# Kernel tuning notes

Measured on AMD Instinct MI355X. Metric: run time of the kernel, lower is better.

The kernel has to match this reference:

```python
import jax, jax.numpy as jnp
import numpy as np
import math

B, T, C = 2, 2048, 1024
H = 16            # n_head
RATIO = 4         # ratio_kv
HKV = H // RATIO  # n_head_kv = 4
HD = C // H       # head_dim = 64
G = H // HKV      # query heads per kv head = 4


def _alibi_slopes(n_heads):
    # n_heads must be a power of 2 here (H=16)
    assert math.log2(n_heads).is_integer()
    start = 2.0 ** (-(2.0 ** (-(math.log2(n_heads) - 3))))
    return np.array([start * (start ** i) for i in range(n_heads)], dtype=np.float32)


def setup_inputs() -> dict:
    key = jax.random.key(0)
    ks = jax.random.split(key, 5)
    return {
        "x": jax.random.normal(ks[0], (B, T, C), dtype=jnp.float32),
        "Wq": jax.random.normal(ks[1], (C, C), dtype=jnp.float32) * 0.02,
        "Wk": jax.random.normal(ks[2], (C, HKV * HD), dtype=jnp.float32) * 0.02,
        "Wv": jax.random.normal(ks[3], (C, HKV * HD), dtype=jnp.float32) * 0.02,
        "Wo": jax.random.normal(ks[4], (C, C), dtype=jnp.float32) * 0.02,
    }


def reference(x, Wq, Wk, Wv, Wo):
    # GQA causal attention with ALiBi bias (flash-disabled fallback path).
    # q: [B,HKV,G,T,HD] (grouped query heads), k/v: [B,HKV,T,HD]
    q = (x @ Wq).reshape(B, T, H, HD).transpose(0, 2, 1, 3).reshape(B, HKV, G, T, HD)
    k = (x @ Wk).reshape(B, T, HKV, HD).transpose(0, 2, 1, 3)
    v = (x @ Wv).reshape(B, T, HKV, HD).transpose(0, 2, 1, 3)

    scale = 1.0 / math.sqrt(HD)
    att = jnp.einsum('bkgtd,bksd->bkgts', q, k) * scale  # [B,HKV,G,T,T]

    # ALiBi: original repeats alibi(n_head) by G and truncates to n_head,
    # so query head h uses slope get_slopes(H)[h // G] == slopes[:HKV] per kv group.
    slopes = jnp.asarray(_alibi_slopes(H))[:HKV]          # [HKV]
    pos = jnp.arange(T)
    rel = (pos[None, :] - pos[:, None]).astype(jnp.float32)  # [T,T], rel[i,j]=j-i
    bias = slopes[:, None, None] * rel                    # [HKV,T,T]
    causal = jnp.triu(jnp.full((T, T), -jnp.inf, dtype=jnp.float32), 1)

    att = att + bias[None, :, None] + causal
    att = jax.nn.softmax(att.astype(jnp.float32), axis=-1).astype(q.dtype)

    y = jnp.einsum('bkgts,bksd->bkgtd', att, v)           # [B,HKV,G,T,HD]
    y = y.reshape(B, H, T, HD).transpose(0, 2, 1, 3).reshape(B, T, C)
    return y @ Wo
```

## Files before the change

### kernel.cpp

```cpp
#include <hip/hip_runtime.h>
#include <hip/hip_bf16.h>
#include <math.h>

#define B_ 2
#define T_ 2048
#define C_ 1024
#define H_ 16
#define HKV_ 4
#define G_ 4
#define HD_ 64
#define KVC_ 256
#define NQKV_ 1536
#define NQT_ 32

typedef __attribute__((ext_vector_type(8))) short bf16x8;
typedef __attribute__((ext_vector_type(4))) float f32x4;

static __device__ inline short f2bf(float f) {
    __hip_bfloat16 h = __float2bfloat16(f);
    short s;
    __builtin_memcpy(&s, &h, 2);
    return s;
}
static __device__ inline short f2bf_trunc(float f) {
    unsigned int u;
    __builtin_memcpy(&u, &f, 4);
    return (short)(u >> 16);
}
static __device__ inline float bf2f(short s) {
    unsigned int u = ((unsigned int)(unsigned short)s) << 16;
    float f;
    __builtin_memcpy(&f, &u, 4);
    return f;
}

static __device__ inline void gload_lds16(const short* g, short* lds) {
    __builtin_amdgcn_global_load_lds(
        (const __attribute__((address_space(1))) unsigned int*)g,
        (__attribute__((address_space(3))) unsigned int*)lds, 16, 0, 0);
}

__global__ __launch_bounds__(256) void cast_bf16(
    const float* __restrict__ in, short* __restrict__ out, int n)
{
    const int i = (blockIdx.x * 256 + threadIdx.x) * 8;
    if (i >= n) return;
    const float4 a = *(const float4*)(in + i);
    const float4 b = *(const float4*)(in + i + 4);
    bf16x8 o;
    o[0] = f2bf(a.x); o[1] = f2bf(a.y); o[2] = f2bf(a.z); o[3] = f2bf(a.w);
    o[4] = f2bf(b.x); o[5] = f2bf(b.y); o[6] = f2bf(b.z); o[7] = f2bf(b.w);
    *(bf16x8*)(out + i) = o;
}

__global__ __launch_bounds__(256) void w_transpose(
    const float* __restrict__ Wq, const float* __restrict__ Wk,
    const float* __restrict__ Wv, const float* __restrict__ Wo,
    short* __restrict__ Wt, short* __restrict__ Wot)
{
    const int z = blockIdx.z;
    const float* in;
    short* out;
    int N;
    if (z == 0)      { in = Wq; out = Wt;                     N = C_; }
    else if (z == 1) { in = Wk; out = Wt + C_ * C_;           N = KVC_; }
    else if (z == 2) { in = Wv; out = Wt + (C_ + KVC_) * C_;  N = KVC_; }
    else             { in = Wo; out = Wot;                    N = C_; }
    const int n0 = blockIdx.x * 32;
    if (n0 >= N) return;
    __shared__ float t[32][33];
    const int tx = threadIdx.x, ty = threadIdx.y;
    const int k0 = blockIdx.y * 32;
    #pragma unroll
    for (int j = 0; j < 4; j++)
        t[ty + j * 8][tx] = in[(size_t)(k0 + ty + j * 8) * N + n0 + tx];
    __syncthreads();
    #pragma unroll
    for (int j = 0; j < 4; j++)
        out[(size_t)(n0 + ty + j * 8) * C_ + k0 + tx] = f2bf(t[tx][ty + j * 8]);
}

template <bool OUT_BF16>
__global__ __launch_bounds__(256) void gemm_bf16(
    const short* __restrict__ A, const short* __restrict__ Bt,
    void* __restrict__ Cout, int M, int N, int K)
{
    __shared__ short As[64 * 32];
    __shared__ short Bs[128 * 32];
    const int tid = threadIdx.x;
    const int wave = tid >> 6, lane = tid & 63;
    const int l15 = lane & 15, quad = lane >> 4;
    const int row0 = blockIdx.y * 64, col0 = blockIdx.x * 128;
    const int wrow = (wave >> 1) * 32, wcol = (wave & 1) * 64;

    f32x4 acc[2][4];
    #pragma unroll
    for (int i = 0; i < 2; i++)
        #pragma unroll
        for (int j = 0; j < 4; j++)
            acc[i][j] = (f32x4){0.f, 0.f, 0.f, 0.f};

    for (int kt = 0; kt < K; kt += 32) {
        __syncthreads();
        {
            const int r = wave * 16 + (lane >> 2);
            const int kof = (lane & 3) * 8;
            gload_lds16(A + (size_t)(row0 + r) * K + kt + kof, &As[wave * 512]);
        }
        #pragma unroll
        for (int c2 = 0; c2 < 2; c2++) {
            const int c = wave * 2 + c2;
            const int r = c * 16 + (lane >> 2);
            const int kof = (lane & 3) * 8;
            gload_lds16(Bt + (size_t)(col0 + r) * K + kt + kof, &Bs[c * 512]);
        }
        __syncthreads();

        bf16x8 af[2], bf[4];
        #pragma unroll
        for (int mt = 0; mt < 2; mt++)
            af[mt] = *(const bf16x8*)&As[(wrow + mt * 16 + l15) * 32 + quad * 8];
        #pragma unroll
        for (int nt = 0; nt < 4; nt++)
            bf[nt] = *(const bf16x8*)&Bs[(wcol + nt * 16 + l15) * 32 + quad * 8];
        #pragma unroll
        for (int mt = 0; mt < 2; mt++)
            #pragma unroll
            for (int nt = 0; nt < 4; nt++)
                acc[mt][nt] = __builtin_amdgcn_mfma_f32_16x16x32_bf16(
                    af[mt], bf[nt], acc[mt][nt], 0, 0, 0);
    }

    #pragma unroll
    for (int mt = 0; mt < 2; mt++) {
        #pragma unroll
        for (int r = 0; r < 4; r++) {
            const size_t row = row0 + wrow + mt * 16 + quad * 4 + r;
            #pragma unroll
            for (int nt = 0; nt < 4; nt++) {
                const size_t col = col0 + wcol + nt * 16 + l15;
                if (OUT_BF16)
                    ((short*)Cout)[row * N + col] = f2bf(acc[mt][nt][r]);
                else
                    ((float*)Cout)[row * N + col] = acc[mt][nt][r];
            }
        }
    }
}

__global__ __launch_bounds__(256) void kv_tile(
    const short* __restrict__ QKV, short* __restrict__ Kt, short* __restrict__ Vt)
{
    __shared__ short Ls[64 * 72];
    const int jt = blockIdx.x;
    const int bk = blockIdx.y;
    const int b = bk >> 2, kh = bk & 3;
    const int tid = threadIdx.x;
    const int key = tid >> 2, d16 = (tid & 3) * 16;
    const size_t src = (size_t)(b * T_ + jt * 64 + key) * NQKV_ + C_ + kh * 64 + d16;
    const size_t tbase = (size_t)(bk * 32 + jt) * 4096;

    {
        const int db0 = (tid & 3) * 2, db1 = db0 + 1;
        *(bf16x8*)(Kt + tbase + key * 64 + ((db0 ^ (key & 7)) * 8)) =
            *(const bf16x8*)(QKV + src);
        *(bf16x8*)(Kt + tbase + key * 64 + ((db1 ^ (key & 7)) * 8)) =
            *(const bf16x8*)(QKV + src + 8);
    }
    *(bf16x8*)&Ls[key * 72 + d16]     = *(const bf16x8*)(QKV + src + KVC_);
    *(bf16x8*)&Ls[key * 72 + d16 + 8] = *(const bf16x8*)(QKV + src + KVC_ + 8);
    __syncthreads();
    const int d = tid >> 2, k16 = (tid & 3) * 16;
    bf16x8 o0, o1;
    #pragma unroll
    for (int i = 0; i < 8; i++) o0[i] = Ls[(k16 + i) * 72 + d];
    #pragma unroll
    for (int i = 0; i < 8; i++) o1[i] = Ls[(k16 + 8 + i) * 72 + d];
    const int kb0 = (tid & 3) * 2, kb1 = kb0 + 1;
    *(bf16x8*)(Vt + tbase + d * 64 + ((kb0 ^ (d & 7)) * 8)) = o0;
    *(bf16x8*)(Vt + tbase + d * 64 + ((kb1 ^ (d & 7)) * 8)) = o1;
}

#define LSTR 72

__global__ __launch_bounds__(256) void attn_mfma(
    const short* __restrict__ QKV, const short* __restrict__ Ktg,
    const short* __restrict__ Vtg, short* __restrict__ Y)
{
    const int qx = blockIdx.x;
    const int bh = blockIdx.y;
    const int qtL = qx, qtH = NQT_ - 1 - qx;
    const int b = bh >> 4, h = bh & 15, kh = h >> 2;
    const float slope2 = exp2f(-0.5f * (float)(kh + 1)) * 1.44269504f;
    const int tid = threadIdx.x;
    const int wave = tid >> 6, lane = tid & 63;
    const int l15 = lane & 15, quad = lane >> 4;
    const int lswz = (l15 & 7) * 8;

    __shared__ short Ks[4096];
    __shared__ short Vs[4096];
    __shared__ short Ps[4 * 32 * LSTR];
    short* Pw = &Ps[wave * 32 * LSTR];
    const int wswz = ((quad >> 1) & 1) << 4;
    const int rswz = ((l15 >> 3) & 1) << 4;

    const size_t bT = (size_t)b * T_;
    const size_t tb0 = (size_t)((b * HKV_ + kh) * 32) * 4096;
    const int qrow0H = qtH * 64 + wave * 16;
    const int qrow0L = qtL * 64 + wave * 16;

    const float qscale = 0.125f * 1.44269504f;
    bf16x8 qfH[2], qfL[2];
    #pragma unroll
    for (int k0 = 0; k0 < 2; k0++) {
        const short* qpH = QKV + (bT + qrow0H + l15) * NQKV_ + h * 64;
        const short* qpL = QKV + (bT + qrow0L + l15) * NQKV_ + h * 64;
        bf16x8 rH = *(const bf16x8*)(qpH + k0 * 32 + quad * 8);
        bf16x8 rL = *(const bf16x8*)(qpL + k0 * 32 + quad * 8);
        #pragma unroll
        for (int j = 0; j < 8; j++) {
            qfH[k0][j] = f2bf(bf2f(rH[j]) * qscale);
            qfL[k0][j] = f2bf(bf2f(rL[j]) * qscale);
        }
    }

    const short one_s = (short)0x3F80;
    const bf16x8 ones = {one_s, one_s, one_s, one_s, one_s, one_s, one_s, one_s};

    f32x4 OaccH[4], OaccL[4], laccH, laccL;
    #pragma unroll
    for (int nt = 0; nt < 4; nt++) {
        OaccH[nt] = (f32x4){0.f, 0.f, 0.f, 0.f};
        OaccL[nt] = (f32x4){0.f, 0.f, 0.f, 0.f};
    }
    laccH = (f32x4){0.f, 0.f, 0.f, 0.f};
    laccL = (f32x4){0.f, 0.f, 0.f, 0.f};

    for (int jtk = 0; jtk <= qtH; jtk++) {
        __syncthreads();
        {
            const short* Ktile = Ktg + tb0 + (size_t)jtk * 4096;
            const short* Vtile = Vtg + tb0 + (size_t)jtk * 4096;
            #pragma unroll
            for (int i = 0; i < 2; i++) {
                const int ch = wave * 2 + i;
                gload_lds16(Ktile + ch * 512 + lane * 8, &Ks[ch * 512]);
                gload_lds16(Vtile + ch * 512 + lane * 8, &Vs[ch * 512]);
            }
        }
        __syncthreads();

        const bool doL = (jtk <= qtL);

        bf16x8 kf[8];
        #pragma unroll
        for (int nt = 0; nt < 4; nt++)
            #pragma unroll
            for (int k0 = 0; k0 < 2; k0++)
                kf[nt * 2 + k0] = *(const bf16x8*)
                    &Ks[(nt * 16 + l15) * 64 + (((k0 * 4 + quad) * 8) ^ lswz)];

        f32x4 sH[4], sL[4];
        #pragma unroll
        for (int nt = 0; nt < 4; nt++) {
            f32x4 a = {0.f, 0.f, 0.f, 0.f};
            a = __builtin_amdgcn_mfma_f32_16x16x32_bf16(qfH[0], kf[nt*2+0], a, 0, 0, 0);
            a = __builtin_amdgcn_mfma_f32_16x16x32_bf16(qfH[1], kf[nt*2+1], a, 0, 0, 0);
            sH[nt] = a;
        }
        if (doL) {
            #pragma unroll
            for (int nt = 0; nt < 4; nt++) {
                f32x4 a = {0.f, 0.f, 0.f, 0.f};
                a = __builtin_amdgcn_mfma_f32_16x16x32_bf16(qfL[0], kf[nt*2+0], a, 0, 0, 0);
                a = __builtin_amdgcn_mfma_f32_16x16x32_bf16(qfL[1], kf[nt*2+1], a, 0, 0, 0);
                sL[nt] = a;
            }
        }

        {
            const float base = slope2 * (float)(jtk * 64 + l15 - quad * 4 - qrow0H);
            if (jtk == qtH) {
                #pragma unroll
                for (int nt = 0; nt < 4; nt++) {
                    const int colsw = ((nt * 16 + l15) ^ wswz);
                    #pragma unroll
                    for (int r = 0; r < 4; r++) {
                        const float relv = (float)(jtk * 64 + l15 - quad * 4 - qrow0H)
                                         + (float)(nt * 16 - r);
                        float p = __builtin_amdgcn_exp2f(
                            fmaf(slope2, (float)(nt * 16 - r), base) + sH[nt][r]);
                        if (relv > 0.f) p = 0.f;
                        Pw[(quad * 4 + r) * LSTR + colsw] = f2bf_trunc(p);
                    }
                }
            } else {
                #pragma unroll
                for (int nt = 0; nt < 4; nt++) {
                    const int colsw = ((nt * 16 + l15) ^ wswz);
                    #pragma unroll
                    for (int r = 0; r < 4; r++) {
                        float p = __builtin_amdgcn_exp2f(
                            fmaf(slope2, (float)(nt * 16 - r), base) + sH[nt][r]);
                        Pw[(quad * 4 + r) * LSTR + colsw] = f2bf_trunc(p);
                    }
                }
            }
        }
        if (doL) {
            const float base = slope2 * (float)(jtk * 64 + l15 - quad * 4 - qrow0L);
            if (jtk == qtL) {
                #pragma unroll
                for (int nt = 0; nt < 4; nt++) {
                    const int colsw = ((nt * 16 + l15) ^ wswz);
                    #pragma unroll
                    for (int r = 0; r < 4; r++) {
                        const float relv = (float)(jtk * 64 + l15 - quad * 4 - qrow0L)
                                         + (float)(nt * 16 - r);
                        float p = __builtin_amdgcn_exp2f(
                            fmaf(slope2, (float)(nt * 16 - r), base) + sL[nt][r]);
                        if (relv > 0.f) p = 0.f;
                        Pw[(16 + quad * 4 + r) * LSTR + colsw] = f2bf_trunc(p);
                    }
                }
            } else {
                #pragma unroll
                for (int nt = 0; nt < 4; nt++) {
                    const int colsw = ((nt * 16 + l15) ^ wswz);
                    #pragma unroll
                    for (int r = 0; r < 4; r++) {
                        float p = __builtin_amdgcn_exp2f(
                            fmaf(slope2, (float)(nt * 16 - r), base) + sL[nt][r]);
                        Pw[(16 + quad * 4 + r) * LSTR + colsw] = f2bf_trunc(p);
                    }
                }
            }
        }
        __asm__ volatile("s_waitcnt lgkmcnt(0)" ::: "memory");

        bf16x8 vf[8];
        #pragma unroll
        for (int nt = 0; nt < 4; nt++)
            #pragma unroll
            for (int k0 = 0; k0 < 2; k0++)
                vf[nt * 2 + k0] = *(const bf16x8*)
                    &Vs[(nt * 16 + l15) * 64 + (((k0 * 4 + quad) * 8) ^ lswz)];

        {
            bf16x8 pf0 = *(const bf16x8*)&Pw[l15 * LSTR + ((quad * 8) ^ rswz)];
            bf16x8 pf1 = *(const bf16x8*)&Pw[l15 * LSTR + ((32 + quad * 8) ^ rswz)];
            laccH = __builtin_amdgcn_mfma_f32_16x16x32_bf16(pf0, ones, laccH, 0, 0, 0);
            laccH = __builtin_amdgcn_mfma_f32_16x16x32_bf16(pf1, ones, laccH, 0, 0, 0);
            #pragma unroll
            for (int nt = 0; nt < 4; nt++) {
                OaccH[nt] = __builtin_amdgcn_mfma_f32_16x16x32_bf16(
                    pf0, vf[nt*2+0], OaccH[nt], 0, 0, 0);
                OaccH[nt] = __builtin_amdgcn_mfma_f32_16x16x32_bf16(
                    pf1, vf[nt*2+1], OaccH[nt], 0, 0, 0);
            }
        }
        if (doL) {
            bf16x8 pf0 = *(const bf16x8*)&Pw[(16 + l15) * LSTR + ((quad * 8) ^ rswz)];
            bf16x8 pf1 = *(const bf16x8*)&Pw[(16 + l15) * LSTR + ((32 + quad * 8) ^ rswz)];
            laccL = __builtin_amdgcn_mfma_f32_16x16x32_bf16(pf0, ones, laccL, 0, 0, 0);
            laccL = __builtin_amdgcn_mfma_f32_16x16x32_bf16(pf1, ones, laccL, 0, 0, 0);
            #pragma unroll
            for (int nt = 0; nt < 4; nt++) {
                OaccL[nt] = __builtin_amdgcn_mfma_f32_16x16x32_bf16(
                    pf0, vf[nt*2+0], OaccL[nt], 0, 0, 0);
                OaccL[nt] = __builtin_amdgcn_mfma_f32_16x16x32_bf16(
                    pf1, vf[nt*2+1], OaccL[nt], 0, 0, 0);
            }
        }
    }

    #pragma unroll
    for (int r = 0; r < 4; r++) {
        const float invH = 1.f / laccH[r];
        const float invL = 1.f / laccL[r];
        const int rowH = qrow0H + quad * 4 + r;
        const int rowL = qrow0L + quad * 4 + r;
        short* ypH = Y + (bT + rowH) * C_ + h * 64 + l15;
        short* ypL = Y + (bT + rowL) * C_ + h * 64 + l15;
        #pragma unroll
        for (int nt = 0; nt < 4; nt++) {
            ypH[nt * 16] = f2bf(OaccH[nt][r] * invH);
            ypL[nt * 16] = f2bf(OaccL[nt][r] * invL);
        }
    }
}

extern "C" void kernel_launch(void* const* d_in, const int* in_sizes, int n_in,
                              void* d_out, int out_size, void* d_ws, size_t ws_size,
                              hipStream_t stream) {
    const float* x  = (const float*)d_in[0];
    const float* Wq = (const float*)d_in[1];
    const float* Wk = (const float*)d_in[2];
    const float* Wv = (const float*)d_in[3];
    const float* Wo = (const float*)d_in[4];
    float* out = (float*)d_out;

    const int M = B_ * T_;
    short* xb  = (short*)d_ws;
    short* Wt  = xb  + (size_t)M * C_;
    short* Wot = Wt  + (size_t)NQKV_ * C_;
    short* QKV = Wot + (size_t)C_ * C_;
    short* Yb  = QKV + (size_t)M * NQKV_;
    short* Ktg = Yb  + (size_t)M * C_;
    short* Vtg = Ktg + (size_t)8 * 32 * 4096;

    cast_bf16<<<dim3(M * C_ / (256 * 8)), dim3(256), 0, stream>>>(x, xb, M * C_);
    w_transpose<<<dim3(32, 32, 4), dim3(32, 8), 0, stream>>>(Wq, Wk, Wv, Wo, Wt, Wot);

    gemm_bf16<true><<<dim3(NQKV_ / 128, M / 64), dim3(256), 0, stream>>>(
        xb, Wt, QKV, M, NQKV_, C_);
    kv_tile<<<dim3(32, 8), dim3(256), 0, stream>>>(QKV, Ktg, Vtg);
    attn_mfma<<<dim3(NQT_ / 2, B_ * H_), dim3(256), 0, stream>>>(QKV, Ktg, Vtg, Yb);
    gemm_bf16<false><<<dim3(C_ / 128, M / 64), dim3(256), 0, stream>>>(
        Yb, Wot, out, M, C_, C_);
}
```

Before: 175.9 us.

## Double-buffer LDS tiles in GEMM and attention with async prefetch

```diff
diff --git a/kernel.cpp b/kernel.cpp
--- a/kernel.cpp
+++ b/kernel.cpp
@@ -85,13 +85,14 @@
     const short* __restrict__ A, const short* __restrict__ Bt,
     void* __restrict__ Cout, int M, int N, int K)
 {
-    __shared__ short As[64 * 32];
-    __shared__ short Bs[128 * 32];
+    __shared__ short As[2][64 * 32];
+    __shared__ short Bs[2][128 * 32];
     const int tid = threadIdx.x;
     const int wave = tid >> 6, lane = tid & 63;
     const int l15 = lane & 15, quad = lane >> 4;
     const int row0 = blockIdx.y * 64, col0 = blockIdx.x * 128;
     const int wrow = (wave >> 1) * 32, wcol = (wave & 1) * 64;
+    const int sr = lane >> 2, kof = (lane & 3) * 8;
 
     f32x4 acc[2][4];
     #pragma unroll
@@ -100,36 +101,43 @@
         for (int j = 0; j < 4; j++)
             acc[i][j] = (f32x4){0.f, 0.f, 0.f, 0.f};
 
-    for (int kt = 0; kt < K; kt += 32) {
-        __syncthreads();
-        {
-            const int r = wave * 16 + (lane >> 2);
-            const int kof = (lane & 3) * 8;
-            gload_lds16(A + (size_t)(row0 + r) * K + kt + kof, &As[wave * 512]);
-        }
-        #pragma unroll
-        for (int c2 = 0; c2 < 2; c2++) {
-            const int c = wave * 2 + c2;
-            const int r = c * 16 + (lane >> 2);
-            const int kof = (lane & 3) * 8;
-            gload_lds16(Bt + (size_t)(col0 + r) * K + kt + kof, &Bs[c * 512]);
-        }
-        __syncthreads();
-
-        bf16x8 af[2], bf[4];
+#define GSTAGE(KT, BUF) do {                                                   \
+        gload_lds16(A + (size_t)(row0 + wave * 16 + sr) * K + (KT) + kof,      \
+                    &As[BUF][wave * 512]);                                     \
+        gload_lds16(Bt + (size_t)(col0 + (wave * 2) * 16 + sr) * K + (KT) + kof,\
+                    &Bs[BUF][(wave * 2) * 512]);                               \
+        gload_lds16(Bt + (size_t)(col0 + (wave * 2 + 1) * 16 + sr) * K + (KT) + kof,\
+                    &Bs[BUF][(wave * 2 + 1) * 512]);                           \
+    } while (0)
+
+    GSTAGE(0, 0);
+    asm volatile("s_waitcnt vmcnt(0)" ::: "memory");
+    __builtin_amdgcn_s_barrier();
+
+    int cur = 0;
+    const int nkt = K >> 5;
+    for (int t = 0; t < nkt; ++t) {
+        if (t + 1 < nkt) GSTAGE((t + 1) * 32, cur ^ 1);
+
+        bf16x8 af[2], bfr[4];
         #pragma unroll
         for (int mt = 0; mt < 2; mt++)
-            af[mt] = *(const bf16x8*)&As[(wrow + mt * 16 + l15) * 32 + quad * 8];
+            af[mt] = *(const bf16x8*)&As[cur][(wrow + mt * 16 + l15) * 32 + quad * 8];
         #pragma unroll
         for (int nt = 0; nt < 4; nt++)
-            bf[nt] = *(const bf16x8*)&Bs[(wcol + nt * 16 + l15) * 32 + quad * 8];
+            bfr[nt] = *(const bf16x8*)&Bs[cur][(wcol + nt * 16 + l15) * 32 + quad * 8];
         #pragma unroll
         for (int mt = 0; mt < 2; mt++)
             #pragma unroll
             for (int nt = 0; nt < 4; nt++)
                 acc[mt][nt] = __builtin_amdgcn_mfma_f32_16x16x32_bf16(
-                    af[mt], bf[nt], acc[mt][nt], 0, 0, 0);
-    }
+                    af[mt], bfr[nt], acc[mt][nt], 0, 0, 0);
+
+        asm volatile("s_waitcnt vmcnt(0)" ::: "memory");
+        __builtin_amdgcn_s_barrier();
+        cur ^= 1;
+    }
+#undef GSTAGE
 
     #pragma unroll
     for (int mt = 0; mt < 2; mt++) {
@@ -197,8 +205,8 @@
     const int l15 = lane & 15, quad = lane >> 4;
     const int lswz = (l15 & 7) * 8;
 
-    __shared__ short Ks[4096];
-    __shared__ short Vs[4096];
+    __shared__ short Ks[2][4096];
+    __shared__ short Vs[2][4096];
     __shared__ short Ps[4 * 32 * LSTR];
     short* Pw = &Ps[wave * 32 * LSTR];
     const int wswz = ((quad >> 1) & 1) << 4;
@@ -236,19 +244,33 @@
     laccH = (f32x4){0.f, 0.f, 0.f, 0.f};
     laccL = (f32x4){0.f, 0.f, 0.f, 0.f};
 
+    {
+        const short* Ktile = Ktg + tb0;
+        const short* Vtile = Vtg + tb0;
+        #pragma unroll
+        for (int i = 0; i < 2; i++) {
+            const int ch = wave * 2 + i;
+            gload_lds16(Ktile + ch * 512 + lane * 8, &Ks[0][ch * 512]);
+            gload_lds16(Vtile + ch * 512 + lane * 8, &Vs[0][ch * 512]);
+        }
+    }
+    asm volatile("s_waitcnt vmcnt(0)" ::: "memory");
+    __builtin_amdgcn_s_barrier();
+
+    int cur = 0;
     for (int jtk = 0; jtk <= qtH; jtk++) {
-        __syncthreads();
-        {
-            const short* Ktile = Ktg + tb0 + (size_t)jtk * 4096;
-            const short* Vtile = Vtg + tb0 + (size_t)jtk * 4096;
+        if (jtk < qtH) {
+            const short* Ktile = Ktg + tb0 + (size_t)(jtk + 1) * 4096;
+            const short* Vtile = Vtg + tb0 + (size_t)(jtk + 1) * 4096;
             #pragma unroll
             for (int i = 0; i < 2; i++) {
                 const int ch = wave * 2 + i;
-                gload_lds16(Ktile + ch * 512 + lane * 8, &Ks[ch * 512]);
-                gload_lds16(Vtile + ch * 512 + lane * 8, &Vs[ch * 512]);
-            }
-        }
-        __syncthreads();
+                gload_lds16(Ktile + ch * 512 + lane * 8, &Ks[cur ^ 1][ch * 512]);
+                gload_lds16(Vtile + ch * 512 + lane * 8, &Vs[cur ^ 1][ch * 512]);
+            }
+        }
+        const short* Ksc = Ks[cur];
+        const short* Vsc = Vs[cur];
 
         const bool doL = (jtk <= qtL);
 
@@ -258,9 +280,10 @@
             #pragma unroll
             for (int k0 = 0; k0 < 2; k0++)
                 kf[nt * 2 + k0] = *(const bf16x8*)
-                    &Ks[(nt * 16 + l15) * 64 + (((k0 * 4 + quad) * 8) ^ lswz)];
+                    &Ksc[(nt * 16 + l15) * 64 + (((k0 * 4 + quad) * 8) ^ lswz)];
 
         f32x4 sH[4], sL[4];
+        __builtin_amdgcn_s_setprio(1);
         #pragma unroll
         for (int nt = 0; nt < 4; nt++) {
             f32x4 a = {0.f, 0.f, 0.f, 0.f};
@@ -277,6 +300,7 @@
                 sL[nt] = a;
             }
         }
+        __builtin_amdgcn_s_setprio(0);
 
         {
             const float base = slope2 * (float)(jtk * 64 + l15 - quad * 4 - qrow0H);
@@ -344,11 +368,12 @@
             #pragma unroll
             for (int k0 = 0; k0 < 2; k0++)
                 vf[nt * 2 + k0] = *(const bf16x8*)
-                    &Vs[(nt * 16 + l15) * 64 + (((k0 * 4 + quad) * 8) ^ lswz)];
+                    &Vsc[(nt * 16 + l15) * 64 + (((k0 * 4 + quad) * 8) ^ lswz)];
 
         {
             bf16x8 pf0 = *(const bf16x8*)&Pw[l15 * LSTR + ((quad * 8) ^ rswz)];
             bf16x8 pf1 = *(const bf16x8*)&Pw[l15 * LSTR + ((32 + quad * 8) ^ rswz)];
+            __builtin_amdgcn_s_setprio(1);
             laccH = __builtin_amdgcn_mfma_f32_16x16x32_bf16(pf0, ones, laccH, 0, 0, 0);
             laccH = __builtin_amdgcn_mfma_f32_16x16x32_bf16(pf1, ones, laccH, 0, 0, 0);
             #pragma unroll
@@ -358,10 +383,12 @@
                 OaccH[nt] = __builtin_amdgcn_mfma_f32_16x16x32_bf16(
                     pf1, vf[nt*2+1], OaccH[nt], 0, 0, 0);
             }
+            __builtin_amdgcn_s_setprio(0);
         }
         if (doL) {
             bf16x8 pf0 = *(const bf16x8*)&Pw[(16 + l15) * LSTR + ((quad * 8) ^ rswz)];
             bf16x8 pf1 = *(const bf16x8*)&Pw[(16 + l15) * LSTR + ((32 + quad * 8) ^ rswz)];
+            __builtin_amdgcn_s_setprio(1);
             laccL = __builtin_amdgcn_mfma_f32_16x16x32_bf16(pf0, ones, laccL, 0, 0, 0);
             laccL = __builtin_amdgcn_mfma_f32_16x16x32_bf16(pf1, ones, laccL, 0, 0, 0);
             #pragma unroll
@@ -371,7 +398,12 @@
                 OaccL[nt] = __builtin_amdgcn_mfma_f32_16x16x32_bf16(
                     pf1, vf[nt*2+1], OaccL[nt], 0, 0, 0);
             }
-        }
+            __builtin_amdgcn_s_setprio(0);
+        }
+
+        asm volatile("s_waitcnt vmcnt(0)" ::: "memory");
+        __builtin_amdgcn_s_barrier();
+        cur ^= 1;
     }
 
     #pragma unroll
```

Measured after the change: 176.7 us. Within noise of the previous version (+0.5%).

## Double-buffer GEMM LDS tiles and enlarge block tile to 128x128

Applied to the files above, without the earlier changes.

```diff
diff --git a/kernel.cpp b/kernel.cpp
--- a/kernel.cpp
+++ b/kernel.cpp
@@ -85,60 +85,70 @@
     const short* __restrict__ A, const short* __restrict__ Bt,
     void* __restrict__ Cout, int M, int N, int K)
 {
-    __shared__ short As[64 * 32];
-    __shared__ short Bs[128 * 32];
+    __shared__ short As[2][128 * 32];
+    __shared__ short Bs[2][128 * 32];
     const int tid = threadIdx.x;
     const int wave = tid >> 6, lane = tid & 63;
     const int l15 = lane & 15, quad = lane >> 4;
-    const int row0 = blockIdx.y * 64, col0 = blockIdx.x * 128;
-    const int wrow = (wave >> 1) * 32, wcol = (wave & 1) * 64;
-
-    f32x4 acc[2][4];
-    #pragma unroll
-    for (int i = 0; i < 2; i++)
+    const int row0 = blockIdx.y * 128, col0 = blockIdx.x * 128;
+    const int wr = (wave >> 1) * 64, wc = (wave & 1) * 64;
+    const int sr = lane >> 2, kof = (lane & 3) * 8;
+
+    f32x4 acc[4][4];
+    #pragma unroll
+    for (int i = 0; i < 4; i++)
         #pragma unroll
         for (int j = 0; j < 4; j++)
             acc[i][j] = (f32x4){0.f, 0.f, 0.f, 0.f};
 
-    for (int kt = 0; kt < K; kt += 32) {
-        __syncthreads();
-        {
-            const int r = wave * 16 + (lane >> 2);
-            const int kof = (lane & 3) * 8;
-            gload_lds16(A + (size_t)(row0 + r) * K + kt + kof, &As[wave * 512]);
-        }
-        #pragma unroll
-        for (int c2 = 0; c2 < 2; c2++) {
-            const int c = wave * 2 + c2;
-            const int r = c * 16 + (lane >> 2);
-            const int kof = (lane & 3) * 8;
-            gload_lds16(Bt + (size_t)(col0 + r) * K + kt + kof, &Bs[c * 512]);
-        }
-        __syncthreads();
-
-        bf16x8 af[2], bf[4];
-        #pragma unroll
-        for (int mt = 0; mt < 2; mt++)
-            af[mt] = *(const bf16x8*)&As[(wrow + mt * 16 + l15) * 32 + quad * 8];
+#define GSTAGE(KT, BUF) do {                                                   \
+        _Pragma("unroll")                                                      \
+        for (int i_ = 0; i_ < 2; i_++) {                                       \
+            const int rr = i_ * 64 + wave * 16;                                \
+            gload_lds16(A + (size_t)(row0 + rr + sr) * K + (KT) + kof,         \
+                        &As[BUF][rr * 32]);                                    \
+            gload_lds16(Bt + (size_t)(col0 + rr + sr) * K + (KT) + kof,        \
+                        &Bs[BUF][rr * 32]);                                    \
+        }                                                                      \
+    } while (0)
+
+    GSTAGE(0, 0);
+    asm volatile("s_waitcnt vmcnt(0)" ::: "memory");
+    __builtin_amdgcn_s_barrier();
+
+    int cur = 0;
+    const int nkt = K >> 5;
+    for (int t = 0; t < nkt; ++t) {
+        if (t + 1 < nkt) GSTAGE((t + 1) * 32, cur ^ 1);
+
+        bf16x8 af[4], bfr[4];
+        #pragma unroll
+        for (int mt = 0; mt < 4; mt++)
+            af[mt] = *(const bf16x8*)&As[cur][(wr + mt * 16 + l15) * 32 + quad * 8];
         #pragma unroll
         for (int nt = 0; nt < 4; nt++)
-            bf[nt] = *(const bf16x8*)&Bs[(wcol + nt * 16 + l15) * 32 + quad * 8];
-        #pragma unroll
-        for (int mt = 0; mt < 2; mt++)
+            bfr[nt] = *(const bf16x8*)&Bs[cur][(wc + nt * 16 + l15) * 32 + quad * 8];
+        #pragma unroll
+        for (int mt = 0; mt < 4; mt++)
             #pragma unroll
             for (int nt = 0; nt < 4; nt++)
                 acc[mt][nt] = __builtin_amdgcn_mfma_f32_16x16x32_bf16(
-                    af[mt], bf[nt], acc[mt][nt], 0, 0, 0);
-    }
-
-    #pragma unroll
-    for (int mt = 0; mt < 2; mt++) {
+                    af[mt], bfr[nt], acc[mt][nt], 0, 0, 0);
+
+        asm volatile("s_waitcnt vmcnt(0)" ::: "memory");
+        __builtin_amdgcn_s_barrier();
+        cur ^= 1;
+    }
+#undef GSTAGE
+
+    #pragma unroll
+    for (int mt = 0; mt < 4; mt++) {
         #pragma unroll
         for (int r = 0; r < 4; r++) {
-            const size_t row = row0 + wrow + mt * 16 + quad * 4 + r;
+            const size_t row = row0 + wr + mt * 16 + quad * 4 + r;
             #pragma unroll
             for (int nt = 0; nt < 4; nt++) {
-                const size_t col = col0 + wcol + nt * 16 + l15;
+                const size_t col = col0 + wc + nt * 16 + l15;
                 if (OUT_BF16)
                     ((short*)Cout)[row * N + col] = f2bf(acc[mt][nt][r]);
                 else
@@ -412,10 +422,10 @@
     cast_bf16<<<dim3(M * C_ / (256 * 8)), dim3(256), 0, stream>>>(x, xb, M * C_);
     w_transpose<<<dim3(32, 32, 4), dim3(32, 8), 0, stream>>>(Wq, Wk, Wv, Wo, Wt, Wot);
 
-    gemm_bf16<true><<<dim3(NQKV_ / 128, M / 64), dim3(256), 0, stream>>>(
+    gemm_bf16<true><<<dim3(NQKV_ / 128, M / 128), dim3(256), 0, stream>>>(
         xb, Wt, QKV, M, NQKV_, C_);
     kv_tile<<<dim3(32, 8), dim3(256), 0, stream>>>(QKV, Ktg, Vtg);
     attn_mfma<<<dim3(NQT_ / 2, B_ * H_), dim3(256), 0, stream>>>(QKV, Ktg, Vtg, Yb);
-    gemm_bf16<false><<<dim3(C_ / 128, M / 64), dim3(256), 0, stream>>>(
+    gemm_bf16<false><<<dim3(C_ / 128, M / 128), dim3(256), 0, stream>>>(
         Yb, Wot, out, M, C_, C_);
 }
```

New measurement: 178.1 us. Within noise of the previous version (+1.3%).
